# Performance work log

Hardware: AMD Instinct MI355X
Metric: run time of the kernel (lower is better)

## Reference

```python
import jax, jax.numpy as jnp
import numpy as np
import math

NUM_LAYERS = 2
D_MODEL = 512
NUM_HEADS = 8
DFF = 2048
TIME_DIM = 8
B = 8
L = 512


def _ffn2(t, w1, b1, w2, b2):
    # gsm_ffn: two Dense(time_dim) layers, both with relu
    h = jax.nn.relu(t @ w1 + b1)
    return jax.nn.relu(h @ w2 + b2)


def _layer_norm(x, g, b, eps=1e-6):
    m = jnp.mean(x, axis=-1, keepdims=True)
    v = jnp.mean(jnp.square(x - m), axis=-1, keepdims=True)
    return (x - m) / jnp.sqrt(v + eps) * g + b


def _forward(x, t, wq, bq, wk, bk, wv, bv, wo, bo, w1, b1, w2, b2,
             ln1g, ln1b, ln2g, ln2b, pw1, pb1, pw2, pb2,
             sw1, sb1, sw2, sb2, bw1, bb1, bw2, bb2):
    Bn, Ln, D = x.shape
    H = NUM_HEADS
    dh = D // H
    scale = jnp.sqrt(jnp.float32(dh))
    two_pi = jnp.float32(2.0 * math.pi)
    for i in range(NUM_LAYERS):
        # ---- TimeGSMKernel: Gibbs spectral-mixture time kernel [B,L,L] ----
        pv = _ffn2(t, pw1[i], pb1[i], pw2[i], pb2[i])            # [B,L,td]
        tp = two_pi * pv * t                                      # [B,L,td]
        cos_enc = jnp.cos(tp[:, :, None, :] - tp[:, None, :, :])  # [B,L,L,td]
        sg = _ffn2(t, sw1[i], sb1[i], sw2[i], sb2[i]) + 1e-6      # [B,L,td]
        sq = sg[:, :, None, :]                                    # [B,L,1,td]
        sk = sg[:, None, :, :]                                    # [B,1,L,td]
        denom = sq * sq + sk * sk
        diff = t[:, :, None, :] - t[:, None, :, :]                # [B,L,L,1]
        exp_enc = jnp.exp(-(diff * diff) / denom)                 # [B,L,L,td]
        local_enc = jnp.sqrt(2.0 * sq * sk / denom)
        be = _ffn2(t, bw1[i], bb1[i], bw2[i], bb2[i])             # [B,L,td]
        kern = jnp.sum(be[:, :, None, :] * be[:, None, :, :]
                       * local_enc * exp_enc * cos_enc, axis=-1)  # [B,L,L]

        # ---- multi-head self-attention with kernel bias ----
        def heads(z):
            return z.reshape(Bn, Ln, H, dh).transpose(0, 2, 1, 3)
        q = heads(x @ wq[i] + bq[i])
        k = heads(x @ wk[i] + bk[i])
        v = heads(x @ wv[i] + bv[i])
        logits = jnp.einsum('bhqd,bhkd->bhqk', q, k) / scale
        logits = logits + (kern / jnp.exp(scale))[:, None, :, :]
        aw = jax.nn.softmax(logits, axis=-1)
        ctx = jnp.einsum('bhqk,bhkd->bhqd', aw, v)
        ctx = ctx.transpose(0, 2, 1, 3).reshape(Bn, Ln, D)
        attn_out = ctx @ wo[i] + bo[i]
        x = _layer_norm(x + attn_out, ln1g[i], ln1b[i])
        # ---- pointwise FFN (relu then linear) ----
        f = jax.nn.relu(x @ w1[i] + b1[i]) @ w2[i] + b2[i]
        x = _layer_norm(x + f, ln2g[i], ln2b[i])
    return x


def setup_inputs() -> dict:
    key = jax.random.key(0)
    ks = iter(jax.random.split(key, 40))
    def nrm(shape, s=0.02):
        return (jax.random.normal(next(ks), shape) * s).astype(jnp.float32)
    NL, D, TD = NUM_LAYERS, D_MODEL, TIME_DIM
    d = {
        'x': jax.random.normal(next(ks), (B, L, D), dtype=jnp.float32),
        't': jax.random.uniform(next(ks), (B, L, 1), dtype=jnp.float32),
        'wq': nrm((NL, D, D)), 'bq': jnp.zeros((NL, D), jnp.float32),
        'wk': nrm((NL, D, D)), 'bk': jnp.zeros((NL, D), jnp.float32),
        'wv': nrm((NL, D, D)), 'bv': jnp.zeros((NL, D), jnp.float32),
        'wo': nrm((NL, D, D)), 'bo': jnp.zeros((NL, D), jnp.float32),
        'w1': nrm((NL, D, DFF)), 'b1': jnp.zeros((NL, DFF), jnp.float32),
        'w2': nrm((NL, DFF, D)), 'b2': jnp.zeros((NL, D), jnp.float32),
        'ln1g': jnp.ones((NL, D), jnp.float32), 'ln1b': jnp.zeros((NL, D), jnp.float32),
        'ln2g': jnp.ones((NL, D), jnp.float32), 'ln2b': jnp.zeros((NL, D), jnp.float32),
        'pw1': nrm((NL, 1, TD), 0.5), 'pb1': 0.1 * jnp.ones((NL, TD), jnp.float32),
        'pw2': nrm((NL, TD, TD), 0.3), 'pb2': 0.1 * jnp.ones((NL, TD), jnp.float32),
        'sw1': nrm((NL, 1, TD), 0.5), 'sb1': 0.1 * jnp.ones((NL, TD), jnp.float32),
        'sw2': nrm((NL, TD, TD), 0.3), 'sb2': 0.5 * jnp.ones((NL, TD), jnp.float32),
        'bw1': nrm((NL, 1, TD), 0.5), 'bb1': 0.1 * jnp.ones((NL, TD), jnp.float32),
        'bw2': nrm((NL, TD, TD), 0.3), 'bb2': 0.1 * jnp.ones((NL, TD), jnp.float32),
    }
    return d


def reference(x, t, wq, bq, wk, bk, wv, bv, wo, bo, w1, b1, w2, b2,
              ln1g, ln1b, ln2g, ln2b, pw1, pb1, pw2, pb2,
              sw1, sb1, sw2, sb2, bw1, bb1, bw2, bb2):
    return _forward(x, t, wq, bq, wk, bk, wv, bv, wo, bo, w1, b1, w2, b2,
                    ln1g, ln1b, ln2g, ln2b, pw1, pb1, pw2, pb2,
                    sw1, sb1, sw2, sb2, bw1, bb1, bw2, bb2)
```

## Files before the change

### kernel.cpp

```cpp
#include <hip/hip_runtime.h>
#include <hip/hip_bf16.h>

#define DEV_INLINE __device__ __forceinline__

constexpr int NLAYERS = 2;
constexpr int DM = 512;
constexpr int NH = 8;
constexpr int DHD = 64;
constexpr int FF = 2048;
constexpr int TD = 8;
constexpr int BB = 8;
constexpr int LL = 512;
constexpr int ROWS = BB * LL;
constexpr int QKVN = 3 * DM;

constexpr float TWO_PI_F = 6.28318530717958647692f;
constexpr float INV_E8 = 3.3546262790251185e-4f;

typedef __attribute__((ext_vector_type(8))) short short8v;
typedef __attribute__((ext_vector_type(4))) float f32x4;

DEV_INLINE unsigned short bf16_rne(float x) {
  unsigned int u = __float_as_uint(x);
  unsigned int r = (u + 0x7fffu + ((u >> 16) & 1u)) >> 16;
  return (unsigned short)r;
}
DEV_INLINE float bf16_to_f(unsigned short h) {
  return __uint_as_float(((unsigned int)h) << 16);
}
DEV_INLINE void split_bf16(float x, unsigned short& h, unsigned short& l) {
  h = bf16_rne(x);
  float lo = x - bf16_to_f(h);
  l = bf16_rne(lo);
}

DEV_INLINE void ffn2_small(float tv,
                           const float* __restrict__ w1, const float* __restrict__ b1,
                           const float* __restrict__ w2, const float* __restrict__ b2,
                           float* out) {
  float h[TD];
#pragma unroll
  for (int d = 0; d < TD; ++d) h[d] = fmaxf(tv * w1[d] + b1[d], 0.f);
#pragma unroll
  for (int j = 0; j < TD; ++j) {
    float acc = b2[j];
#pragma unroll
    for (int d = 0; d < TD; ++d) acc += h[d] * w2[d * TD + j];
    out[j] = fmaxf(acc, 0.f);
  }
}

__global__ __launch_bounds__(256) void small_ffn_kernel(
    const float* __restrict__ t,
    const float* __restrict__ pw1, const float* __restrict__ pb1,
    const float* __restrict__ pw2, const float* __restrict__ pb2,
    const float* __restrict__ sw1, const float* __restrict__ sb1,
    const float* __restrict__ sw2, const float* __restrict__ sb2,
    const float* __restrict__ bw1, const float* __restrict__ bb1,
    const float* __restrict__ bw2, const float* __restrict__ bb2,
    float* __restrict__ tp, float* __restrict__ sg, float* __restrict__ be) {
  const int i = blockIdx.x * 256 + threadIdx.x;
  if (i >= ROWS) return;
  const float tv = t[i];
  float o[TD];
  ffn2_small(tv, pw1, pb1, pw2, pb2, o);
#pragma unroll
  for (int d = 0; d < TD; ++d) tp[(size_t)i * TD + d] = TWO_PI_F * o[d] * tv;
  ffn2_small(tv, sw1, sb1, sw2, sb2, o);
#pragma unroll
  for (int d = 0; d < TD; ++d) sg[(size_t)i * TD + d] = o[d] + 1e-6f;
  ffn2_small(tv, bw1, bb1, bw2, bb2, o);
#pragma unroll
  for (int d = 0; d < TD; ++d) be[(size_t)i * TD + d] = o[d];
}

DEV_INLINE void load8(const float* __restrict__ p, float* o) {
  float4 a = *reinterpret_cast<const float4*>(p);
  float4 b = *reinterpret_cast<const float4*>(p + 4);
  o[0] = a.x; o[1] = a.y; o[2] = a.z; o[3] = a.w;
  o[4] = b.x; o[5] = b.y; o[6] = b.z; o[7] = b.w;
}

__global__ __launch_bounds__(256) void kern_kernel(
    const float* __restrict__ t, const float* __restrict__ tp,
    const float* __restrict__ sg, const float* __restrict__ be,
    float* __restrict__ kernS) {
  const int k = blockIdx.x * 256 + threadIdx.x;
  const int q = blockIdx.y;
  const int b = blockIdx.z;
  const size_t iq = (size_t)b * LL + q;
  const size_t ik = (size_t)b * LL + k;
  const float tq = t[iq], tk = t[ik];
  const float diff = tq - tk;
  const float d2 = diff * diff;

  float tpq[TD], sgq[TD], beq[TD], tpk[TD], sgk[TD], bek[TD];
  load8(tp + iq * TD, tpq);
  load8(sg + iq * TD, sgq);
  load8(be + iq * TD, beq);
  load8(tp + ik * TD, tpk);
  load8(sg + ik * TD, sgk);
  load8(be + ik * TD, bek);

  float acc = 0.f;
#pragma unroll
  for (int d = 0; d < TD; ++d) {
    const float sq = sgq[d], sk = sgk[d];
    const float denom = sq * sq + sk * sk;
    const float inv = 1.0f / denom;
    const float e = __expf(-d2 * inv);
    const float loc = sqrtf(2.0f * sq * sk * inv);
    const float c = __cosf(tpq[d] - tpk[d]);
    acc += beq[d] * bek[d] * loc * e * c;
  }
  kernS[((size_t)b * LL + q) * LL + k] = acc * INV_E8;
}

__global__ __launch_bounds__(256) void td_kernel(
    const float* __restrict__ W, unsigned short* __restrict__ Thi,
    unsigned short* __restrict__ Tlo, int K, int N) {
  __shared__ float tile[32][33];
  const int k0 = blockIdx.x * 32, n0 = blockIdx.y * 32;
  const int tx = threadIdx.x & 31, ty = threadIdx.x >> 5;
#pragma unroll
  for (int i = 0; i < 4; ++i)
    tile[ty + i * 8][tx] = W[(size_t)(k0 + ty + i * 8) * N + n0 + tx];
  __syncthreads();
#pragma unroll
  for (int i = 0; i < 4; ++i) {
    const int n = n0 + ty + i * 8;
    const float v = tile[tx][ty + i * 8];
    unsigned short h, l;
    split_bf16(v, h, l);
    Thi[(size_t)n * K + k0 + tx] = h;
    Tlo[(size_t)n * K + k0 + tx] = l;
  }
}

__global__ __launch_bounds__(256) void decomp_kernel(
    const float* __restrict__ X, unsigned short* __restrict__ Hi,
    unsigned short* __restrict__ Lo, int n4) {
  const int i = blockIdx.x * 256 + threadIdx.x;
  if (i >= n4) return;
  const float4 v = *reinterpret_cast<const float4*>(X + (size_t)i * 4);
  unsigned short h0, h1, h2, h3, l0, l1, l2, l3;
  split_bf16(v.x, h0, l0);
  split_bf16(v.y, h1, l1);
  split_bf16(v.z, h2, l2);
  split_bf16(v.w, h3, l3);
  uint2 hv, lv;
  hv.x = (unsigned)h0 | ((unsigned)h1 << 16);
  hv.y = (unsigned)h2 | ((unsigned)h3 << 16);
  lv.x = (unsigned)l0 | ((unsigned)l1 << 16);
  lv.y = (unsigned)l2 | ((unsigned)l3 << 16);
  *reinterpret_cast<uint2*>(Hi + (size_t)i * 4) = hv;
  *reinterpret_cast<uint2*>(Lo + (size_t)i * 4) = lv;
}

__global__ __launch_bounds__(256) void qkvbias_kernel(
    const float* __restrict__ bq, const float* __restrict__ bk,
    const float* __restrict__ bv, float* __restrict__ out) {
  const int i = blockIdx.x * 256 + threadIdx.x;
  if (i >= QKVN) return;
  out[i] = i < DM ? bq[i] : (i < 2 * DM ? bk[i - DM] : bv[i - 2 * DM]);
}

template <int BN, bool RELU, bool SPLIT_OUT>
__global__ __launch_bounds__(256) void gemm_mfma(
    const unsigned short* __restrict__ Ahi, const unsigned short* __restrict__ Alo,
    const unsigned short* __restrict__ Bhi, const unsigned short* __restrict__ Blo,
    const float* __restrict__ bias, float* __restrict__ C,
    unsigned short* __restrict__ Chi, unsigned short* __restrict__ Clo,
    int M, int N, int K) {
  constexpr int BM = 128, BK = 64;
  constexpr int WT_M = 64;
  constexpr int WT_N = BN / 2;
  constexpr int MI = WT_M / 16;
  constexpr int NI = WT_N / 16;
  constexpr int A_IT = BM * BK / (256 * 8);
  constexpr int B_IT = BN * BK / (256 * 8);

  __shared__ unsigned short AsH[2][BM * BK];
  __shared__ unsigned short AsL[2][BM * BK];
  __shared__ unsigned short BsH[2][BN * BK];
  __shared__ unsigned short BsL[2][BN * BK];

  const int nwg = gridDim.x * gridDim.y;
  const int orig = blockIdx.y * gridDim.x + blockIdx.x;
  const int swz = (orig & 7) * (nwg >> 3) + (orig >> 3);
  const int bx = swz % gridDim.x;
  const int by = swz / gridDim.x;

  const int tid = threadIdx.x;
  const int lane = tid & 63;
  const int wid = tid >> 6;
  const int wr = wid >> 1, wc = wid & 1;
  const int rowBase = by * BM;
  const int colBase = bx * BN;
  const int l15 = lane & 15, l4 = lane >> 4;

  const int sg_ = tid & 7;
  const int srA = tid >> 3;
  const int swg = sg_ ^ (srA & 7);

  f32x4 acc[MI][NI] = {};
  const int nt = K / BK;

  uint4 ahR[A_IT], alR[A_IT], bhR[B_IT], blR[B_IT];

  auto loadRegs = [&](int kt) {
    const int k0 = kt * BK;
#pragma unroll
    for (int it = 0; it < A_IT; ++it) {
      const size_t base = (size_t)(rowBase + it * 32 + srA) * K + k0 + sg_ * 8;
      ahR[it] = *reinterpret_cast<const uint4*>(Ahi + base);
      alR[it] = *reinterpret_cast<const uint4*>(Alo + base);
    }
#pragma unroll
    for (int it = 0; it < B_IT; ++it) {
      const size_t base = (size_t)(colBase + it * 32 + srA) * K + k0 + sg_ * 8;
      bhR[it] = *reinterpret_cast<const uint4*>(Bhi + base);
      blR[it] = *reinterpret_cast<const uint4*>(Blo + base);
    }
  };

  auto writeLDS = [&](int buf) {
#pragma unroll
    for (int it = 0; it < A_IT; ++it) {
      const int off = ((it * 32 + srA) << 6) + (swg << 3);
      *reinterpret_cast<uint4*>(&AsH[buf][off]) = ahR[it];
      *reinterpret_cast<uint4*>(&AsL[buf][off]) = alR[it];
    }
#pragma unroll
    for (int it = 0; it < B_IT; ++it) {
      const int off = ((it * 32 + srA) << 6) + (swg << 3);
      *reinterpret_cast<uint4*>(&BsH[buf][off]) = bhR[it];
      *reinterpret_cast<uint4*>(&BsL[buf][off]) = blR[it];
    }
  };

  loadRegs(0);
  writeLDS(0);
  if (nt > 1) loadRegs(1);

  for (int t = 0; t < nt; ++t) {
    __syncthreads();
    const int cur = t & 1;
    if (t + 1 < nt) writeLDS(cur ^ 1);
    if (t + 2 < nt) loadRegs(t + 2);

#pragma unroll
    for (int ks = 0; ks < 2; ++ks) {
      short8v ah[MI], al[MI], bh[NI], bl[NI];
#pragma unroll
      for (int mi = 0; mi < MI; ++mi) {
        const int r = wr * WT_M + mi * 16 + l15;
        const int off = (r << 6) + (((ks * 4 + l4) ^ (r & 7)) << 3);
        ah[mi] = *reinterpret_cast<const short8v*>(&AsH[cur][off]);
        al[mi] = *reinterpret_cast<const short8v*>(&AsL[cur][off]);
      }
#pragma unroll
      for (int ni = 0; ni < NI; ++ni) {
        const int r = wc * WT_N + ni * 16 + l15;
        const int off = (r << 6) + (((ks * 4 + l4) ^ (r & 7)) << 3);
        bh[ni] = *reinterpret_cast<const short8v*>(&BsH[cur][off]);
        bl[ni] = *reinterpret_cast<const short8v*>(&BsL[cur][off]);
      }
#pragma unroll
      for (int mi = 0; mi < MI; ++mi)
#pragma unroll
        for (int ni = 0; ni < NI; ++ni) {
          acc[mi][ni] = __builtin_amdgcn_mfma_f32_16x16x32_bf16(ah[mi], bh[ni], acc[mi][ni], 0, 0, 0);
          acc[mi][ni] = __builtin_amdgcn_mfma_f32_16x16x32_bf16(al[mi], bh[ni], acc[mi][ni], 0, 0, 0);
          acc[mi][ni] = __builtin_amdgcn_mfma_f32_16x16x32_bf16(ah[mi], bl[ni], acc[mi][ni], 0, 0, 0);
        }
    }
  }

#pragma unroll
  for (int mi = 0; mi < MI; ++mi) {
#pragma unroll
    for (int ni = 0; ni < NI; ++ni) {
      const int col = colBase + wc * WT_N + ni * 16 + l15;
      const float bv = bias[col];
#pragma unroll
      for (int j = 0; j < 4; ++j) {
        const int row = rowBase + wr * WT_M + mi * 16 + l4 * 4 + j;
        float v = acc[mi][ni][j] + bv;
        if (RELU) v = fmaxf(v, 0.f);
        if (SPLIT_OUT) {
          unsigned short h, l;
          split_bf16(v, h, l);
          Chi[(size_t)row * N + col] = h;
          Clo[(size_t)row * N + col] = l;
        } else {
          C[(size_t)row * N + col] = v;
        }
      }
    }
  }
}

__global__ __launch_bounds__(256) void txp_kernel(
    const float* __restrict__ qkvb, float* __restrict__ ktb) {
  __shared__ float tile[32][33];
  const int bh = blockIdx.z;
  const int b = bh >> 3, h = bh & 7;
  const int kk0 = blockIdx.x * 32, d0 = blockIdx.y * 32;
  const int tx = threadIdx.x & 31, ty = threadIdx.x >> 5;
#pragma unroll
  for (int i = 0; i < 4; ++i) {
    const int kk = kk0 + ty + i * 8;
    tile[ty + i * 8][tx] = qkvb[(size_t)(b * LL + kk) * QKVN + DM + h * DHD + d0 + tx];
  }
  __syncthreads();
#pragma unroll
  for (int i = 0; i < 4; ++i) {
    const int d = d0 + ty + i * 8;
    ktb[((size_t)bh * DHD + d) * LL + kk0 + tx] = tile[tx][ty + i * 8];
  }
}

constexpr int TQ = 8;

__global__ __launch_bounds__(256) void attn_kernel(
    const float* __restrict__ qkvb, const float* __restrict__ ktb,
    const float* __restrict__ kernS,
    unsigned short* __restrict__ ctxhi, unsigned short* __restrict__ ctxlo) {
  const int qt = blockIdx.x;
  const int h = blockIdx.y;
  const int b = blockIdx.z;
  const int tid = threadIdx.x;
  const int q0 = qt * TQ;

  __shared__ float qst[DHD][TQ];
  __shared__ float lst[LL][TQ];
  __shared__ float red[4][TQ][DHD];
  __shared__ float invS[TQ];

  {
    const int d = tid & 63;
    const int qq0 = tid >> 6;
#pragma unroll
    for (int rep = 0; rep < 2; ++rep) {
      const int qq = qq0 + rep * 4;
      qst[d][qq] = qkvb[(size_t)(b * LL + q0 + qq) * QKVN + h * DHD + d];
    }
  }
  __syncthreads();

  {
    const int kk = tid;
    const float* kcol = ktb + (size_t)(b * NH + h) * DHD * LL;
    float dot0[TQ] = {}, dot1[TQ] = {};
#pragma unroll 4
    for (int d = 0; d < DHD; ++d) {
      const float ka = kcol[(size_t)d * LL + kk];
      const float kb2 = kcol[(size_t)d * LL + kk + 256];
      const float4 qa = *reinterpret_cast<const float4*>(&qst[d][0]);
      const float4 qb2 = *reinterpret_cast<const float4*>(&qst[d][4]);
      dot0[0] += qa.x * ka; dot0[1] += qa.y * ka; dot0[2] += qa.z * ka; dot0[3] += qa.w * ka;
      dot0[4] += qb2.x * ka; dot0[5] += qb2.y * ka; dot0[6] += qb2.z * ka; dot0[7] += qb2.w * ka;
      dot1[0] += qa.x * kb2; dot1[1] += qa.y * kb2; dot1[2] += qa.z * kb2; dot1[3] += qa.w * kb2;
      dot1[4] += qb2.x * kb2; dot1[5] += qb2.y * kb2; dot1[6] += qb2.z * kb2; dot1[7] += qb2.w * kb2;
    }
#pragma unroll
    for (int qq = 0; qq < TQ; ++qq) {
      const size_t kbase = ((size_t)b * LL + q0 + qq) * LL;
      lst[kk][qq] = dot0[qq] * 0.125f + kernS[kbase + kk];
      lst[kk + 256][qq] = dot1[qq] * 0.125f + kernS[kbase + kk + 256];
    }
  }
  __syncthreads();

  {
    const int row = tid >> 5;
    const int l32 = tid & 31;
    float m = -1e30f;
#pragma unroll
    for (int j = 0; j < 16; ++j) m = fmaxf(m, lst[l32 + j * 32][row]);
#pragma unroll
    for (int s = 16; s; s >>= 1) m = fmaxf(m, __shfl_xor(m, s, 32));
    float sum = 0.f;
#pragma unroll
    for (int j = 0; j < 16; ++j) {
      const float e = __expf(lst[l32 + j * 32][row] - m);
      lst[l32 + j * 32][row] = e;
      sum += e;
    }
#pragma unroll
    for (int s = 16; s; s >>= 1) sum += __shfl_xor(sum, s, 32);
    if (l32 == 0) invS[row] = 1.0f / sum;
  }
  __syncthreads();

  const int d = tid & 63;
  const int c = tid >> 6;
  float acc[TQ] = {};
  for (int kk = c * 128; kk < c * 128 + 128; ++kk) {
    const float vv = qkvb[(size_t)(b * LL + kk) * QKVN + 2 * DM + h * DHD + d];
    const float4 pa = *reinterpret_cast<const float4*>(&lst[kk][0]);
    const float4 pb2 = *reinterpret_cast<const float4*>(&lst[kk][4]);
    acc[0] += pa.x * vv; acc[1] += pa.y * vv; acc[2] += pa.z * vv; acc[3] += pa.w * vv;
    acc[4] += pb2.x * vv; acc[5] += pb2.y * vv; acc[6] += pb2.z * vv; acc[7] += pb2.w * vv;
  }
#pragma unroll
  for (int qq = 0; qq < TQ; ++qq) red[c][qq][d] = acc[qq];
  __syncthreads();
  if (c == 0) {
#pragma unroll
    for (int qq = 0; qq < TQ; ++qq) {
      const float r = ((red[0][qq][d] + red[1][qq][d]) + (red[2][qq][d] + red[3][qq][d])) * invS[qq];
      unsigned short hh, ll;
      split_bf16(r, hh, ll);
      const size_t o = (size_t)(b * LL + q0 + qq) * DM + h * DHD + d;
      ctxhi[o] = hh;
      ctxlo[o] = ll;
    }
  }
}

__global__ __launch_bounds__(256) void resid_ln_kernel(
    const float* __restrict__ X, const float* __restrict__ R,
    const float* __restrict__ g, const float* __restrict__ bta,
    float* __restrict__ Out, unsigned short* __restrict__ OutHi,
    unsigned short* __restrict__ OutLo) {
  const int row = blockIdx.x * 4 + (threadIdx.x >> 6);
  const int lane = threadIdx.x & 63;
  const float* x = X + (size_t)row * DM;
  const float* r = R + (size_t)row * DM;

  float v[8];
  float s = 0.f;
#pragma unroll
  for (int j = 0; j < 2; ++j) {
    const float4 a = *reinterpret_cast<const float4*>(x + lane * 8 + j * 4);
    const float4 c = *reinterpret_cast<const float4*>(r + lane * 8 + j * 4);
    v[j * 4 + 0] = a.x + c.x;
    v[j * 4 + 1] = a.y + c.y;
    v[j * 4 + 2] = a.z + c.z;
    v[j * 4 + 3] = a.w + c.w;
    s += v[j * 4 + 0] + v[j * 4 + 1] + v[j * 4 + 2] + v[j * 4 + 3];
  }
#pragma unroll
  for (int m = 1; m < 64; m <<= 1) s += __shfl_xor(s, m, 64);
  const float mean = s * (1.f / DM);
  float var = 0.f;
#pragma unroll
  for (int j = 0; j < 8; ++j) {
    const float dlt = v[j] - mean;
    var += dlt * dlt;
  }
#pragma unroll
  for (int m = 1; m < 64; m <<= 1) var += __shfl_xor(var, m, 64);
  var *= (1.f / DM);
  const float inv = 1.0f / sqrtf(var + 1e-6f);

  unsigned short hs[8], ls[8];
#pragma unroll
  for (int j = 0; j < 2; ++j) {
    const float4 gg = *reinterpret_cast<const float4*>(g + lane * 8 + j * 4);
    const float4 bb = *reinterpret_cast<const float4*>(bta + lane * 8 + j * 4);
    float4 o;
    o.x = (v[j * 4 + 0] - mean) * inv * gg.x + bb.x;
    o.y = (v[j * 4 + 1] - mean) * inv * gg.y + bb.y;
    o.z = (v[j * 4 + 2] - mean) * inv * gg.z + bb.z;
    o.w = (v[j * 4 + 3] - mean) * inv * gg.w + bb.w;
    *reinterpret_cast<float4*>(Out + (size_t)row * DM + lane * 8 + j * 4) = o;
    split_bf16(o.x, hs[j * 4 + 0], ls[j * 4 + 0]);
    split_bf16(o.y, hs[j * 4 + 1], ls[j * 4 + 1]);
    split_bf16(o.z, hs[j * 4 + 2], ls[j * 4 + 2]);
    split_bf16(o.w, hs[j * 4 + 3], ls[j * 4 + 3]);
  }
  uint4 hv, lv;
  hv.x = (unsigned)hs[0] | ((unsigned)hs[1] << 16);
  hv.y = (unsigned)hs[2] | ((unsigned)hs[3] << 16);
  hv.z = (unsigned)hs[4] | ((unsigned)hs[5] << 16);
  hv.w = (unsigned)hs[6] | ((unsigned)hs[7] << 16);
  lv.x = (unsigned)ls[0] | ((unsigned)ls[1] << 16);
  lv.y = (unsigned)ls[2] | ((unsigned)ls[3] << 16);
  lv.z = (unsigned)ls[4] | ((unsigned)ls[5] << 16);
  lv.w = (unsigned)ls[6] | ((unsigned)ls[7] << 16);
  *reinterpret_cast<uint4*>(OutHi + (size_t)row * DM + lane * 8) = hv;
  *reinterpret_cast<uint4*>(OutLo + (size_t)row * DM + lane * 8) = lv;
}

extern "C" void kernel_launch(void* const* d_in, const int* in_sizes, int n_in,
                              void* d_out, int out_size, void* d_ws, size_t ws_size,
                              hipStream_t stream) {
  const float* x_in = (const float*)d_in[0];
  const float* t = (const float*)d_in[1];
  const float* wq = (const float*)d_in[2];
  const float* bq = (const float*)d_in[3];
  const float* wk = (const float*)d_in[4];
  const float* bk = (const float*)d_in[5];
  const float* wv = (const float*)d_in[6];
  const float* bv = (const float*)d_in[7];
  const float* wo = (const float*)d_in[8];
  const float* bo = (const float*)d_in[9];
  const float* w1 = (const float*)d_in[10];
  const float* b1 = (const float*)d_in[11];
  const float* w2 = (const float*)d_in[12];
  const float* b2 = (const float*)d_in[13];
  const float* ln1g = (const float*)d_in[14];
  const float* ln1b = (const float*)d_in[15];
  const float* ln2g = (const float*)d_in[16];
  const float* ln2b = (const float*)d_in[17];
  const float* pw1 = (const float*)d_in[18];
  const float* pb1 = (const float*)d_in[19];
  const float* pw2 = (const float*)d_in[20];
  const float* pb2 = (const float*)d_in[21];
  const float* sw1 = (const float*)d_in[22];
  const float* sb1 = (const float*)d_in[23];
  const float* sw2 = (const float*)d_in[24];
  const float* sb2 = (const float*)d_in[25];
  const float* bw1 = (const float*)d_in[26];
  const float* bb1 = (const float*)d_in[27];
  const float* bw2 = (const float*)d_in[28];
  const float* bb2 = (const float*)d_in[29];

  char* wsb = (char*)d_ws;
  size_t off = 0;
  auto allocB = [&](size_t bytes) {
    char* p = wsb + off;
    off += (bytes + 255) & ~(size_t)255;
    return p;
  };
  float* tpb = (float*)allocB(ROWS * TD * 4);
  float* sgb = (float*)allocB(ROWS * TD * 4);
  float* beb = (float*)allocB(ROWS * TD * 4);
  float* kernS = (float*)allocB((size_t)BB * LL * LL * 4);
  float* qkvb = (float*)allocB((size_t)ROWS * QKVN * 4);
  float* ktb = (float*)allocB((size_t)BB * NH * DHD * LL * 4);
  float* ao = (float*)allocB((size_t)ROWS * DM * 4);
  float* xb = (float*)allocB((size_t)ROWS * DM * 4);
  float* fb = (float*)allocB((size_t)ROWS * DM * 4);
  float* xn = (float*)allocB((size_t)ROWS * DM * 4);
  float* qkvbias = (float*)allocB(QKVN * 4);
  unsigned short* qkvwt_hi = (unsigned short*)allocB((size_t)QKVN * DM * 2);
  unsigned short* qkvwt_lo = (unsigned short*)allocB((size_t)QKVN * DM * 2);
  unsigned short* wot_hi = (unsigned short*)allocB((size_t)DM * DM * 2);
  unsigned short* wot_lo = (unsigned short*)allocB((size_t)DM * DM * 2);
  unsigned short* w1t_hi = (unsigned short*)allocB((size_t)FF * DM * 2);
  unsigned short* w1t_lo = (unsigned short*)allocB((size_t)FF * DM * 2);
  unsigned short* w2t_hi = (unsigned short*)allocB((size_t)DM * FF * 2);
  unsigned short* w2t_lo = (unsigned short*)allocB((size_t)DM * FF * 2);
  unsigned short* xhi = (unsigned short*)allocB((size_t)ROWS * DM * 2);
  unsigned short* xlo = (unsigned short*)allocB((size_t)ROWS * DM * 2);
  unsigned short* ctxhi = (unsigned short*)allocB((size_t)ROWS * DM * 2);
  unsigned short* ctxlo = (unsigned short*)allocB((size_t)ROWS * DM * 2);
  unsigned short* hhi = (unsigned short*)qkvb;
  unsigned short* hlo = hhi + (size_t)ROWS * FF;

  const float* xcur = x_in;

  for (int i = 0; i < NLAYERS; ++i) {
    td_kernel<<<dim3(16, 16), 256, 0, stream>>>(wq + (size_t)i * DM * DM, qkvwt_hi, qkvwt_lo, DM, DM);
    td_kernel<<<dim3(16, 16), 256, 0, stream>>>(wk + (size_t)i * DM * DM, qkvwt_hi + (size_t)DM * DM, qkvwt_lo + (size_t)DM * DM, DM, DM);
    td_kernel<<<dim3(16, 16), 256, 0, stream>>>(wv + (size_t)i * DM * DM, qkvwt_hi + (size_t)2 * DM * DM, qkvwt_lo + (size_t)2 * DM * DM, DM, DM);
    td_kernel<<<dim3(16, 16), 256, 0, stream>>>(wo + (size_t)i * DM * DM, wot_hi, wot_lo, DM, DM);
    td_kernel<<<dim3(16, 64), 256, 0, stream>>>(w1 + (size_t)i * DM * FF, w1t_hi, w1t_lo, DM, FF);
    td_kernel<<<dim3(64, 16), 256, 0, stream>>>(w2 + (size_t)i * FF * DM, w2t_hi, w2t_lo, FF, DM);
    qkvbias_kernel<<<(QKVN + 255) / 256, 256, 0, stream>>>(bq + i * DM, bk + i * DM, bv + i * DM, qkvbias);

    small_ffn_kernel<<<ROWS / 256, 256, 0, stream>>>(
        t, pw1 + i * TD, pb1 + i * TD, pw2 + i * TD * TD, pb2 + i * TD,
        sw1 + i * TD, sb1 + i * TD, sw2 + i * TD * TD, sb2 + i * TD,
        bw1 + i * TD, bb1 + i * TD, bw2 + i * TD * TD, bb2 + i * TD,
        tpb, sgb, beb);
    kern_kernel<<<dim3(LL / 256, LL, BB), 256, 0, stream>>>(t, tpb, sgb, beb, kernS);

    if (i == 0) {
      decomp_kernel<<<(ROWS * DM / 4 + 255) / 256, 256, 0, stream>>>(x_in, xhi, xlo, ROWS * DM / 4);
    }

    gemm_mfma<128, false, false><<<dim3(QKVN / 128, ROWS / 128), 256, 0, stream>>>(
        xhi, xlo, qkvwt_hi, qkvwt_lo, qkvbias, qkvb, nullptr, nullptr, ROWS, QKVN, DM);

    txp_kernel<<<dim3(LL / 32, DHD / 32, BB * NH), 256, 0, stream>>>(qkvb, ktb);

    attn_kernel<<<dim3(LL / TQ, NH, BB), 256, 0, stream>>>(qkvb, ktb, kernS, ctxhi, ctxlo);

    gemm_mfma<64, false, false><<<dim3(DM / 64, ROWS / 128), 256, 0, stream>>>(
        ctxhi, ctxlo, wot_hi, wot_lo, bo + i * DM, ao, nullptr, nullptr, ROWS, DM, DM);

    resid_ln_kernel<<<ROWS / 4, 256, 0, stream>>>(
        xcur, ao, ln1g + i * DM, ln1b + i * DM, xb, xhi, xlo);

    gemm_mfma<128, true, true><<<dim3(FF / 128, ROWS / 128), 256, 0, stream>>>(
        xhi, xlo, w1t_hi, w1t_lo, b1 + i * FF, nullptr, hhi, hlo, ROWS, FF, DM);

    gemm_mfma<64, false, false><<<dim3(DM / 64, ROWS / 128), 256, 0, stream>>>(
        hhi, hlo, w2t_hi, w2t_lo, b2 + i * DM, fb, nullptr, nullptr, ROWS, DM, FF);

    float* ln2_out = (i == NLAYERS - 1) ? (float*)d_out : xn;
    resid_ln_kernel<<<ROWS / 4, 256, 0, stream>>>(
        xb, fb, ln2g + i * DM, ln2b + i * DM, ln2_out, xhi, xlo);

    xcur = xn;
  }
}
```

Baseline: 922.8 us.

## Single-buffer GEMM LDS and restructure attention into 512-thread blocks with register softmax

The GEMM drops LDS double buffering for a single buffer with an extra barrier per k-tile. This halves shared memory use, which could raise occupancy, but it serializes the LDS writes with compute. The attention kernel now uses 512 threads, one key per thread, and does the softmax in registers with wave shuffles. It also remaps block indices with a swizzle so co-scheduled blocks share K/V for a batch, and splits the PV reduction 8 ways. These changes touch several unrelated aspects and carry opposite risks.

```diff
diff --git a/kernel.cpp b/kernel.cpp
--- a/kernel.cpp
+++ b/kernel.cpp
@@ -180,10 +180,10 @@
   constexpr int A_IT = BM * BK / (256 * 8);
   constexpr int B_IT = BN * BK / (256 * 8);
 
-  __shared__ unsigned short AsH[2][BM * BK];
-  __shared__ unsigned short AsL[2][BM * BK];
-  __shared__ unsigned short BsH[2][BN * BK];
-  __shared__ unsigned short BsL[2][BN * BK];
+  __shared__ unsigned short AsH[BM * BK];
+  __shared__ unsigned short AsL[BM * BK];
+  __shared__ unsigned short BsH[BN * BK];
+  __shared__ unsigned short BsL[BN * BK];
 
   const int nwg = gridDim.x * gridDim.y;
   const int orig = blockIdx.y * gridDim.x + blockIdx.x;
@@ -224,30 +224,27 @@
     }
   };
 
-  auto writeLDS = [&](int buf) {
+  auto writeLDS = [&]() {
 #pragma unroll
     for (int it = 0; it < A_IT; ++it) {
       const int off = ((it * 32 + srA) << 6) + (swg << 3);
-      *reinterpret_cast<uint4*>(&AsH[buf][off]) = ahR[it];
-      *reinterpret_cast<uint4*>(&AsL[buf][off]) = alR[it];
+      *reinterpret_cast<uint4*>(&AsH[off]) = ahR[it];
+      *reinterpret_cast<uint4*>(&AsL[off]) = alR[it];
     }
 #pragma unroll
     for (int it = 0; it < B_IT; ++it) {
       const int off = ((it * 32 + srA) << 6) + (swg << 3);
-      *reinterpret_cast<uint4*>(&BsH[buf][off]) = bhR[it];
-      *reinterpret_cast<uint4*>(&BsL[buf][off]) = blR[it];
+      *reinterpret_cast<uint4*>(&BsH[off]) = bhR[it];
+      *reinterpret_cast<uint4*>(&BsL[off]) = blR[it];
     }
   };
 
   loadRegs(0);
-  writeLDS(0);
-  if (nt > 1) loadRegs(1);
 
   for (int t = 0; t < nt; ++t) {
+    writeLDS();
     __syncthreads();
-    const int cur = t & 1;
-    if (t + 1 < nt) writeLDS(cur ^ 1);
-    if (t + 2 < nt) loadRegs(t + 2);
+    if (t + 1 < nt) loadRegs(t + 1);
 
 #pragma unroll
     for (int ks = 0; ks < 2; ++ks) {
@@ -256,15 +253,15 @@
       for (int mi = 0; mi < MI; ++mi) {
         const int r = wr * WT_M + mi * 16 + l15;
         const int off = (r << 6) + (((ks * 4 + l4) ^ (r & 7)) << 3);
-        ah[mi] = *reinterpret_cast<const short8v*>(&AsH[cur][off]);
-        al[mi] = *reinterpret_cast<const short8v*>(&AsL[cur][off]);
+        ah[mi] = *reinterpret_cast<const short8v*>(&AsH[off]);
+        al[mi] = *reinterpret_cast<const short8v*>(&AsL[off]);
       }
 #pragma unroll
       for (int ni = 0; ni < NI; ++ni) {
         const int r = wc * WT_N + ni * 16 + l15;
         const int off = (r << 6) + (((ks * 4 + l4) ^ (r & 7)) << 3);
-        bh[ni] = *reinterpret_cast<const short8v*>(&BsH[cur][off]);
-        bl[ni] = *reinterpret_cast<const short8v*>(&BsL[cur][off]);
+        bh[ni] = *reinterpret_cast<const short8v*>(&BsH[off]);
+        bl[ni] = *reinterpret_cast<const short8v*>(&BsL[off]);
       }
 #pragma unroll
       for (int mi = 0; mi < MI; ++mi)
@@ -275,6 +272,7 @@
           acc[mi][ni] = __builtin_amdgcn_mfma_f32_16x16x32_bf16(ah[mi], bl[ni], acc[mi][ni], 0, 0, 0);
         }
     }
+    if (t + 1 < nt) __syncthreads();
   }
 
 #pragma unroll
@@ -323,86 +321,112 @@
 
 constexpr int TQ = 8;
 
-__global__ __launch_bounds__(256) void attn_kernel(
+__global__ __launch_bounds__(512) void attn_kernel(
     const float* __restrict__ qkvb, const float* __restrict__ ktb,
     const float* __restrict__ kernS,
     unsigned short* __restrict__ ctxhi, unsigned short* __restrict__ ctxlo) {
-  const int qt = blockIdx.x;
-  const int h = blockIdx.y;
-  const int b = blockIdx.z;
+  const int id = blockIdx.x + 8 * (blockIdx.y + 64 * blockIdx.z);
+  const int w = (id & 7) * 512 + (id >> 3);
+  const int h = w & 7;
+  const int qt = (w >> 3) & 63;
+  const int b = w >> 9;
   const int tid = threadIdx.x;
   const int q0 = qt * TQ;
 
   __shared__ float qst[DHD][TQ];
-  __shared__ float lst[LL][TQ];
-  __shared__ float red[4][TQ][DHD];
-  __shared__ float invS[TQ];
+  __shared__ float lst[LL][12];
+  __shared__ float red[8][TQ][DHD];
+  __shared__ float wred[8][TQ];
+  __shared__ float gmax[TQ], ginv[TQ];
 
   {
-    const int d = tid & 63;
-    const int qq0 = tid >> 6;
-#pragma unroll
-    for (int rep = 0; rep < 2; ++rep) {
-      const int qq = qq0 + rep * 4;
-      qst[d][qq] = qkvb[(size_t)(b * LL + q0 + qq) * QKVN + h * DHD + d];
-    }
-  }
-  __syncthreads();
-
+    const int qq = tid & 7, d = tid >> 3;
+    qst[d][qq] = qkvb[(size_t)(b * LL + q0 + qq) * QKVN + h * DHD + d];
+  }
+  __syncthreads();
+
+  const int kk = tid;
+  float dot[TQ] = {};
   {
-    const int kk = tid;
-    const float* kcol = ktb + (size_t)(b * NH + h) * DHD * LL;
-    float dot0[TQ] = {}, dot1[TQ] = {};
-#pragma unroll 4
+    const float* kcol = ktb + (size_t)(b * NH + h) * DHD * LL + kk;
+#pragma unroll 8
     for (int d = 0; d < DHD; ++d) {
-      const float ka = kcol[(size_t)d * LL + kk];
-      const float kb2 = kcol[(size_t)d * LL + kk + 256];
+      const float ka = kcol[(size_t)d * LL];
       const float4 qa = *reinterpret_cast<const float4*>(&qst[d][0]);
-      const float4 qb2 = *reinterpret_cast<const float4*>(&qst[d][4]);
-      dot0[0] += qa.x * ka; dot0[1] += qa.y * ka; dot0[2] += qa.z * ka; dot0[3] += qa.w * ka;
-      dot0[4] += qb2.x * ka; dot0[5] += qb2.y * ka; dot0[6] += qb2.z * ka; dot0[7] += qb2.w * ka;
-      dot1[0] += qa.x * kb2; dot1[1] += qa.y * kb2; dot1[2] += qa.z * kb2; dot1[3] += qa.w * kb2;
-      dot1[4] += qb2.x * kb2; dot1[5] += qb2.y * kb2; dot1[6] += qb2.z * kb2; dot1[7] += qb2.w * kb2;
-    }
-#pragma unroll
-    for (int qq = 0; qq < TQ; ++qq) {
-      const size_t kbase = ((size_t)b * LL + q0 + qq) * LL;
-      lst[kk][qq] = dot0[qq] * 0.125f + kernS[kbase + kk];
-      lst[kk + 256][qq] = dot1[qq] * 0.125f + kernS[kbase + kk + 256];
-    }
-  }
-  __syncthreads();
+      const float4 qb = *reinterpret_cast<const float4*>(&qst[d][4]);
+      dot[0] += qa.x * ka; dot[1] += qa.y * ka; dot[2] += qa.z * ka; dot[3] += qa.w * ka;
+      dot[4] += qb.x * ka; dot[5] += qb.y * ka; dot[6] += qb.z * ka; dot[7] += qb.w * ka;
+    }
+    const size_t kbase = ((size_t)b * LL + q0) * LL + kk;
+#pragma unroll
+    for (int qq = 0; qq < TQ; ++qq)
+      dot[qq] = dot[qq] * 0.125f + kernS[kbase + (size_t)qq * LL];
+  }
+
+  const int lane = tid & 63;
+  const int wv = tid >> 6;
 
   {
-    const int row = tid >> 5;
-    const int l32 = tid & 31;
-    float m = -1e30f;
-#pragma unroll
-    for (int j = 0; j < 16; ++j) m = fmaxf(m, lst[l32 + j * 32][row]);
-#pragma unroll
-    for (int s = 16; s; s >>= 1) m = fmaxf(m, __shfl_xor(m, s, 32));
-    float sum = 0.f;
-#pragma unroll
-    for (int j = 0; j < 16; ++j) {
-      const float e = __expf(lst[l32 + j * 32][row] - m);
-      lst[l32 + j * 32][row] = e;
-      sum += e;
-    }
-#pragma unroll
-    for (int s = 16; s; s >>= 1) sum += __shfl_xor(sum, s, 32);
-    if (l32 == 0) invS[row] = 1.0f / sum;
+    float mv[TQ];
+#pragma unroll
+    for (int qq = 0; qq < TQ; ++qq) mv[qq] = dot[qq];
+#pragma unroll
+    for (int s = 1; s < 64; s <<= 1)
+#pragma unroll
+      for (int qq = 0; qq < TQ; ++qq) mv[qq] = fmaxf(mv[qq], __shfl_xor(mv[qq], s, 64));
+    if (lane == 0) {
+#pragma unroll
+      for (int qq = 0; qq < TQ; ++qq) wred[wv][qq] = mv[qq];
+    }
+  }
+  __syncthreads();
+  if (tid < TQ) {
+    float m = wred[0][tid];
+#pragma unroll
+    for (int w2 = 1; w2 < 8; ++w2) m = fmaxf(m, wred[w2][tid]);
+    gmax[tid] = m;
+  }
+  __syncthreads();
+
+  {
+    float sv[TQ];
+#pragma unroll
+    for (int qq = 0; qq < TQ; ++qq) sv[qq] = __expf(dot[qq] - gmax[qq]);
+    float4 p0, p1;
+    p0.x = sv[0]; p0.y = sv[1]; p0.z = sv[2]; p0.w = sv[3];
+    p1.x = sv[4]; p1.y = sv[5]; p1.z = sv[6]; p1.w = sv[7];
+    *reinterpret_cast<float4*>(&lst[kk][0]) = p0;
+    *reinterpret_cast<float4*>(&lst[kk][4]) = p1;
+#pragma unroll
+    for (int s = 1; s < 64; s <<= 1)
+#pragma unroll
+      for (int qq = 0; qq < TQ; ++qq) sv[qq] += __shfl_xor(sv[qq], s, 64);
+    if (lane == 0) {
+#pragma unroll
+      for (int qq = 0; qq < TQ; ++qq) wred[wv][qq] = sv[qq];
+    }
+  }
+  __syncthreads();
+  if (tid < TQ) {
+    float s = wred[0][tid];
+#pragma unroll
+    for (int w2 = 1; w2 < 8; ++w2) s += wred[w2][tid];
+    ginv[tid] = 1.0f / s;
   }
   __syncthreads();
 
   const int d = tid & 63;
   const int c = tid >> 6;
   float acc[TQ] = {};
-  for (int kk = c * 128; kk < c * 128 + 128; ++kk) {
-    const float vv = qkvb[(size_t)(b * LL + kk) * QKVN + 2 * DM + h * DHD + d];
-    const float4 pa = *reinterpret_cast<const float4*>(&lst[kk][0]);
-    const float4 pb2 = *reinterpret_cast<const float4*>(&lst[kk][4]);
-    acc[0] += pa.x * vv; acc[1] += pa.y * vv; acc[2] += pa.z * vv; acc[3] += pa.w * vv;
-    acc[4] += pb2.x * vv; acc[5] += pb2.y * vv; acc[6] += pb2.z * vv; acc[7] += pb2.w * vv;
+  {
+    const float* vbase = qkvb + (size_t)(b * LL) * QKVN + 2 * DM + h * DHD + d;
+    for (int k2 = c * 64; k2 < c * 64 + 64; ++k2) {
+      const float vvv = vbase[(size_t)k2 * QKVN];
+      const float4 pa = *reinterpret_cast<const float4*>(&lst[k2][0]);
+      const float4 pb = *reinterpret_cast<const float4*>(&lst[k2][4]);
+      acc[0] += pa.x * vvv; acc[1] += pa.y * vvv; acc[2] += pa.z * vvv; acc[3] += pa.w * vvv;
+      acc[4] += pb.x * vvv; acc[5] += pb.y * vvv; acc[6] += pb.z * vvv; acc[7] += pb.w * vvv;
+    }
   }
 #pragma unroll
   for (int qq = 0; qq < TQ; ++qq) red[c][qq][d] = acc[qq];
@@ -410,7 +434,10 @@
   if (c == 0) {
 #pragma unroll
     for (int qq = 0; qq < TQ; ++qq) {
-      const float r = ((red[0][qq][d] + red[1][qq][d]) + (red[2][qq][d] + red[3][qq][d])) * invS[qq];
+      float r = red[0][qq][d];
+#pragma unroll
+      for (int cc = 1; cc < 8; ++cc) r += red[cc][qq][d];
+      r *= ginv[qq];
       unsigned short hh, ll;
       split_bf16(r, hh, ll);
       const size_t o = (size_t)(b * LL + q0 + qq) * DM + h * DHD + d;
@@ -579,7 +606,7 @@
 
     txp_kernel<<<dim3(LL / 32, DHD / 32, BB * NH), 256, 0, stream>>>(qkvb, ktb);
 
-    attn_kernel<<<dim3(LL / TQ, NH, BB), 256, 0, stream>>>(qkvb, ktb, kernS, ctxhi, ctxlo);
+    attn_kernel<<<dim3(NH, LL / TQ, BB), 512, 0, stream>>>(qkvb, ktb, kernS, ctxhi, ctxlo);
 
     gemm_mfma<64, false, false><<<dim3(DM / 64, ROWS / 128), 256, 0, stream>>>(
         ctxhi, ctxlo, wot_hi, wot_lo, bo + i * DM, ao, nullptr, nullptr, ROWS, DM, DM);
```

After: 1.148 ms. 1.24x slower.
